# Optimization experiments

Measured on AMD Instinct MI355X. Metric: run time of the kernel, lower is better.

## Reference

```python
import jax, jax.numpy as jnp
import numpy as np

IN_CH = 64
EMBED = 128
OUT_CH = 64
NUM_HEADS = 2
HEAD_DIM = EMBED // NUM_HEADS
B, D, H, W = 2, 16, 16, 16
SEQ = D * H * W


def setup_inputs() -> dict:
    key = jax.random.key(0)
    ks = jax.random.split(key, 12)
    s = lambda fan_in: 1.0 / np.sqrt(fan_in)
    return {
        "x": jax.random.normal(ks[0], (B, IN_CH, D, H, W), dtype=jnp.float32),
        "W_cp": jax.random.uniform(ks[1], (EMBED, IN_CH), jnp.float32, -s(IN_CH), s(IN_CH)),
        "b_cp": jax.random.uniform(ks[2], (EMBED,), jnp.float32, -s(IN_CH), s(IN_CH)),
        "W_q": jax.random.uniform(ks[3], (EMBED, EMBED), jnp.float32, -s(EMBED), s(EMBED)),
        "W_k": jax.random.uniform(ks[4], (EMBED, EMBED), jnp.float32, -s(EMBED), s(EMBED)),
        "W_v": jax.random.uniform(ks[5], (EMBED, EMBED), jnp.float32, -s(EMBED), s(EMBED)),
        "W_o": jax.random.uniform(ks[6], (EMBED, EMBED), jnp.float32, -s(EMBED), s(EMBED)),
        "b_o": jax.random.uniform(ks[7], (EMBED,), jnp.float32, -s(EMBED), s(EMBED)),
        "W_out": jax.random.uniform(ks[8], (OUT_CH, EMBED), jnp.float32, -s(EMBED), s(EMBED)),
        "b_out": jax.random.uniform(ks[9], (OUT_CH,), jnp.float32, -s(EMBED), s(EMBED)),
        "pos": jax.random.normal(ks[10], (1, SEQ, EMBED), dtype=jnp.float32) * 0.02,
        "gate": jnp.float32(0.1),
    }


def reference(x, W_cp, b_cp, W_q, W_k, W_v, W_o, b_o, W_out, b_out, pos, gate):
    b, c, d, h, w = x.shape
    seq = d * h * w
    scale = HEAD_DIM ** (-0.5)
    # (B, C, D, H, W) -> (B, S, C)
    xf = jnp.transpose(x, (0, 2, 3, 4, 1)).reshape(b, seq, c)
    xf = xf @ W_cp.T + b_cp + pos  # (B, S, E)
    # QKV projections, split heads: (B, nh, S, hd)
    def heads(t):
        return jnp.transpose(t.reshape(b, seq, NUM_HEADS, HEAD_DIM), (0, 2, 1, 3))
    q = heads(xf @ W_q.T)
    k = heads(xf @ W_k.T)
    v = heads(xf @ W_v.T)
    attn = jax.nn.softmax(jnp.einsum("bnsd,bntd->bnst", q, k) * scale, axis=-1)
    o = jnp.einsum("bnst,bntd->bnsd", attn, v)  # (B, nh, S, hd)
    o = jnp.transpose(o, (0, 2, 1, 3)).reshape(b, seq, EMBED)
    o = o @ W_o.T + b_o
    o = o @ W_out.T + b_out  # (B, S, out)
    out = jnp.transpose(o, (0, 2, 1)).reshape(b, OUT_CH, d, h, w)
    # in_channels == output_dim -> skip is identity (no conv/BN in original)
    return out + gate * x
```

## Files before the change

### kernel.cpp

```cpp
#include <hip/hip_runtime.h>
#include <hip/hip_bf16.h>
#include <cstdint>

typedef unsigned short u16;
typedef __attribute__((ext_vector_type(8))) short short8;
typedef __attribute__((ext_vector_type(8))) float f32x8;
typedef __attribute__((ext_vector_type(4))) float f32x4;

#define MFMA(a, b, c) __builtin_amdgcn_mfma_f32_16x16x32_bf16((a), (b), (c), 0, 0, 0)

#define SEQ 4096
#define KSPLIT 8
#define NTILE (SEQ / KSPLIT / 32)

static __device__ __forceinline__ float b2f(u16 u) {
    union { float f; uint32_t i; } c; c.i = ((uint32_t)u) << 16; return c.f;
}
static __device__ __forceinline__ u16 f2b(float f) {
    union { float f; uint32_t i; } c; c.f = f;
    uint32_t r = c.i + 0x7FFF + ((c.i >> 16) & 1);
    return (u16)(r >> 16);
}
static __device__ __forceinline__ short8 ld8(const u16* p) {
    return *reinterpret_cast<const short8*>(p);
}
static __device__ __forceinline__ uint32_t pk2(float a, float b) {
    uint32_t r;
    asm("v_cvt_pk_bf16_f32 %0, %1, %2" : "=v"(r) : "v"(a), "v"(b));
    return r;
}
static __device__ __forceinline__ void gld16(const u16* g, u16* l) {
    __builtin_amdgcn_global_load_lds(
        (const __attribute__((address_space(1))) unsigned int*)g,
        (__attribute__((address_space(3))) unsigned int*)l, 16, 0, 0);
}

__global__ void k_prep(const float* __restrict__ Wo, const float* __restrict__ bo,
                       const float* __restrict__ Wout, const float* __restrict__ bout,
                       const float* __restrict__ Wcp, const float* __restrict__ Wq,
                       const float* __restrict__ Wk, const float* __restrict__ Wv,
                       u16* __restrict__ Wc, float* __restrict__ bc,
                       u16* __restrict__ Wcp_b, u16* __restrict__ Wq_b,
                       u16* __restrict__ Wk_b, u16* __restrict__ Wv_b) {
    int idx = blockIdx.x * 256 + threadIdx.x;
    if (idx < 8192) {
        int co = idx >> 7, e = idx & 127;
        float s = 0.f;
        for (int k = 0; k < 128; k++)
            s += Wout[co * 128 + k] * Wo[k * 128 + e];
        Wc[idx] = f2b(s);
    } else if (idx < 8256) {
        int co = idx - 8192;
        float s = bout[co];
        for (int k = 0; k < 128; k++)
            s += bo[k] * Wout[co * 128 + k];
        bc[co] = s;
    } else if (idx < 16448) {
        int i = idx - 8256;  Wcp_b[i] = f2b(Wcp[i]);
    } else if (idx < 32832) {
        int i = idx - 16448; Wq_b[i] = f2b(Wq[i]);
    } else if (idx < 49216) {
        int i = idx - 32832; Wk_b[i] = f2b(Wk[i]);
    } else if (idx < 65600) {
        int i = idx - 49216; Wv_b[i] = f2b(Wv[i]);
    }
}

__global__ __launch_bounds__(256) void k_front(const float* __restrict__ x,
                                               const u16* __restrict__ Wcp,
                                               const float* __restrict__ bcp,
                                               const float* __restrict__ pos,
                                               const u16* __restrict__ Wq,
                                               const u16* __restrict__ Wk,
                                               const u16* __restrict__ Wv,
                                               u16* __restrict__ Q, u16* __restrict__ K,
                                               u16* __restrict__ V) {
    __shared__ __align__(16) u16 xT[32][72];
    __shared__ __align__(16) u16 xfl[32 * 128];
    int blk = blockIdx.x;
    int b = blk >> 7, sb = (blk & 127) * 32;
    int t = threadIdx.x, w = t >> 6, l = t & 63, lc = l & 15, lg = l >> 4;

    {
        int c = t & 63, so = t >> 6;
        const float* src = x + ((size_t)b * 64 + c) * SEQ + sb + so * 8;
        f32x8 a0 = *reinterpret_cast<const f32x8*>(src);
#pragma unroll
        for (int j = 0; j < 8; j++) xT[so * 8 + j][c] = f2b(a0[j]);
    }
    __syncthreads();

    {
        int rt = w >> 1, eh = w & 1;
        short8 af[2];
        af[0] = ld8(&xT[rt * 16 + lc][lg * 8]);
        af[1] = ld8(&xT[rt * 16 + lc][32 + lg * 8]);
#pragma unroll
        for (int et = 0; et < 4; et++) {
            int nt = eh * 4 + et;
            f32x4 acc = {0.f, 0.f, 0.f, 0.f};
#pragma unroll
            for (int ks = 0; ks < 2; ks++) {
                short8 bfr = ld8(Wcp + (nt * 16 + lc) * 64 + ks * 32 + lg * 8);
                acc = MFMA(af[ks], bfr, acc);
            }
            int e = nt * 16 + lc;
            float be = bcp[e];
            int chunk = e >> 3;
#pragma unroll
            for (int r = 0; r < 4; r++) {
                int sl = rt * 16 + lg * 4 + r;
                float v = acc[r] + be + pos[(size_t)(sb + sl) * 128 + e];
                xfl[sl * 128 + ((chunk ^ (sl & 7)) << 3) + (e & 7)] = f2b(v);
            }
        }
    }
    __syncthreads();

    {
        int st = w & 1, hr = w >> 1;
        short8 afq[4];
#pragma unroll
        for (int ks = 0; ks < 4; ks++)
            afq[ks] = ld8(&xfl[(st * 16 + lc) * 128 + (((ks * 4 + lg) ^ (lc & 7)) << 3)]);

        const float qscl = 0.18033688011112042f;
#pragma unroll
        for (int qk = 0; qk < 2; qk++) {
            const u16* W = qk ? Wk : Wq;
            u16* dst = qk ? K : Q;
#pragma unroll
            for (int et = 0; et < 4; et++) {
                int nt = hr * 4 + et;
                f32x4 acc = {0.f, 0.f, 0.f, 0.f};
#pragma unroll
                for (int ks = 0; ks < 4; ks++) {
                    short8 bfr = ld8(W + (nt * 16 + lc) * 128 + ks * 32 + lg * 8);
                    acc = MFMA(afq[ks], bfr, acc);
                }
                int e = nt * 16 + lc, h = e >> 6, d = e & 63;
                float scl = qk ? 1.0f : qscl;
#pragma unroll
                for (int r = 0; r < 4; r++) {
                    int sr = sb + st * 16 + lg * 4 + r;
                    dst[(((size_t)b * 2 + h) * SEQ + sr) * 64 + d] = f2b(acc[r] * scl);
                }
            }
        }
#pragma unroll
        for (int et = 0; et < 4; et++) {
            int nt = hr * 4 + et;
            f32x4 acc = {0.f, 0.f, 0.f, 0.f};
            short8 wv[4];
#pragma unroll
            for (int ks = 0; ks < 4; ks++)
                wv[ks] = ld8(Wv + (nt * 16 + lc) * 128 + ks * 32 + lg * 8);
#pragma unroll
            for (int ks = 0; ks < 4; ks++)
                acc = MFMA(wv[ks], afq[ks], acc);
#pragma unroll
            for (int r = 0; r < 4; r++) {
                int d = nt * 16 + lg * 4 + r, h = d >> 6, dd = d & 63;
                V[((size_t)(b * 2 + h) * 64 + dd) * SEQ + sb + st * 16 + lc] = f2b(acc[r]);
            }
        }
    }
}

__global__ __launch_bounds__(256, 4) void k_attn(const u16* __restrict__ Q,
                                                 const u16* __restrict__ K,
                                                 const u16* __restrict__ Vg,
                                                 u16* __restrict__ Op,
                                                 float2* __restrict__ ml) {
    __shared__ __align__(16) u16 Klds[2][2048];
    __shared__ __align__(16) u16 Vlds[2][2048];
    __shared__ __align__(16) u16 Pl[4][32][32];
    int blk = blockIdx.x;
    int split = blk >> 7, bh = (blk >> 5) & 3, qb = (blk & 31) * 128;
    int kbase = split * (SEQ / KSPLIT);
    const u16* Qp = Q + (size_t)bh * SEQ * 64;
    const u16* Kp = K + (size_t)bh * SEQ * 64;
    const u16* Vp = Vg + (size_t)bh * SEQ * 64;
    int t = threadIdx.x, w = t >> 6, l = t & 63, lc = l & 15, lg = l >> 4;
    uint32_t* plw = (uint32_t*)&Pl[w][0][0];
    const u16* plu = &Pl[w][0][0];

    const u16* kSrc = Kp + (size_t)(kbase + w * 8 + (l >> 3)) * 64 + (((l & 7) ^ (l >> 3)) << 3);
    int vrow = w * 16 + (l >> 2);
    int vswz = (l & 3) ^ ((((l >> 2) & 3) + (l >> 4)) & 3);
    const u16* vSrc = Vp + (size_t)vrow * SEQ + kbase + (vswz << 3);

    short8 qa[2][2];
#pragma unroll
    for (int ks = 0; ks < 2; ks++)
#pragma unroll
        for (int qh = 0; qh < 2; qh++)
            qa[ks][qh] = ld8(Qp + (size_t)(qb + w * 32 + qh * 16 + lc) * 64 + ks * 32 + lg * 8);

    short8 onesb;
#pragma unroll
    for (int i = 0; i < 8; i++) onesb[i] = (short)0x3F80;

    f32x4 oacc[2][4], lsacc[2];
#pragma unroll
    for (int qh = 0; qh < 2; qh++) {
        lsacc[qh] = (f32x4){0.f, 0.f, 0.f, 0.f};
#pragma unroll
        for (int dt = 0; dt < 4; dt++) oacc[qh][dt] = (f32x4){0.f, 0.f, 0.f, 0.f};
    }
    float m[2] = {-INFINITY, -INFINITY};

    int c0 = (lg ^ (lc & 7)) * 8;
    int sp = (((lc & 3) + (lc >> 2)) & 3);
    int cv = (lg ^ sp) * 8;

#define STAGE(buf, tt) do {                                       \
        gld16(kSrc + (size_t)(tt) * 2048, &Klds[buf][w * 512]);   \
        gld16(vSrc + (tt) * 32,           &Vlds[buf][w * 512]);   \
    } while (0)

    STAGE(0, 0);
    __syncthreads();

#pragma unroll 2
    for (int tt = 0; tt < NTILE; tt++) {
        int cur = tt & 1;
        if (tt + 1 < NTILE) STAGE(cur ^ 1, tt + 1);

        const u16* kb = Klds[cur];
        const u16* vb = Vlds[cur];

        f32x4 sc[2][2];
#pragma unroll
        for (int nt = 0; nt < 2; nt++) {
            short8 kf0 = ld8(kb + (nt * 16 + lc) * 64 + c0);
            short8 kf1 = ld8(kb + (nt * 16 + lc) * 64 + (c0 ^ 32));
#pragma unroll
            for (int qh = 0; qh < 2; qh++) {
                f32x4 a = {0.f, 0.f, 0.f, 0.f};
                a = MFMA(kf0, qa[0][qh], a);
                a = MFMA(kf1, qa[1][qh], a);
                sc[nt][qh] = a;
            }
        }

        float mx[2];
#pragma unroll
        for (int qh = 0; qh < 2; qh++)
            mx[qh] = fmaxf(
                fmaxf(fmaxf(sc[0][qh][0], sc[0][qh][1]), fmaxf(sc[0][qh][2], sc[0][qh][3])),
                fmaxf(fmaxf(sc[1][qh][0], sc[1][qh][1]), fmaxf(sc[1][qh][2], sc[1][qh][3])));

        if (__any((mx[0] - m[0] > 8.f) || (mx[1] - m[1] > 8.f))) {
#pragma unroll
            for (int qh = 0; qh < 2; qh++) {
                float mr = fmaxf(mx[qh], __shfl_xor(mx[qh], 16));
                mr = fmaxf(mr, __shfl_xor(mr, 32));
                float mn = fmaxf(m[qh], mr);
                float corr = exp2f(m[qh] - mn);
#pragma unroll
                for (int r = 0; r < 4; r++) {
                    float cr = __shfl(corr, lg * 4 + r);
#pragma unroll
                    for (int dt = 0; dt < 4; dt++) oacc[qh][dt][r] *= cr;
                    lsacc[qh][r] *= cr;
                }
                m[qh] = mn;
            }
        }

#pragma unroll
        for (int qh = 0; qh < 2; qh++) {
            int rowb = (qh * 16 + lc) * 16 + (lg & 1) * 2;
#pragma unroll
            for (int nt = 0; nt < 2; nt++) {
                uint2 u;
                u.x = pk2(exp2f(sc[nt][qh][0] - m[qh]), exp2f(sc[nt][qh][1] - m[qh]));
                u.y = pk2(exp2f(sc[nt][qh][2] - m[qh]), exp2f(sc[nt][qh][3] - m[qh]));
                int cc = (nt * 2 + (lg >> 1)) ^ sp;
                *reinterpret_cast<uint2*>(&plw[rowb + cc * 4]) = u;
            }
        }

        short8 pa0 = ld8(plu + (lc) * 32 + cv);
        short8 pa1 = ld8(plu + (16 + lc) * 32 + cv);
        lsacc[0] = MFMA(pa0, onesb, lsacc[0]);
        lsacc[1] = MFMA(pa1, onesb, lsacc[1]);
#pragma unroll
        for (int dt = 0; dt < 4; dt++) {
            short8 vf = ld8(vb + (dt * 16 + lc) * 32 + cv);
            oacc[0][dt] = MFMA(pa0, vf, oacc[0][dt]);
            oacc[1][dt] = MFMA(pa1, vf, oacc[1][dt]);
        }
        __syncthreads();
    }
#undef STAGE

    size_t rowbase = (size_t)(split * 4 + bh) * SEQ + qb + w * 32;
#pragma unroll
    for (int qh = 0; qh < 2; qh++)
#pragma unroll
        for (int dt = 0; dt < 4; dt++)
#pragma unroll
            for (int r = 0; r < 4; r++)
                Op[(rowbase + qh * 16 + lg * 4 + r) * 64 + dt * 16 + lc] = f2b(oacc[qh][dt][r]);
    float mr[2][4];
#pragma unroll
    for (int qh = 0; qh < 2; qh++)
#pragma unroll
        for (int r = 0; r < 4; r++) mr[qh][r] = __shfl(m[qh], lg * 4 + r);
    if (lc == 0) {
#pragma unroll
        for (int qh = 0; qh < 2; qh++)
#pragma unroll
            for (int r = 0; r < 4; r++) {
                float2 v; v.x = mr[qh][r]; v.y = lsacc[qh][r];
                ml[rowbase + qh * 16 + lg * 4 + r] = v;
            }
    }
}

__global__ __launch_bounds__(256) void k_back(const u16* __restrict__ Op,
                                              const float2* __restrict__ ml,
                                              const u16* __restrict__ Wc,
                                              const float* __restrict__ bc,
                                              const float* __restrict__ x,
                                              const float* __restrict__ gate,
                                              float* __restrict__ out) {
    __shared__ __align__(16) u16 Ol[32 * 128];
    int blk = blockIdx.x;
    int b = blk >> 7, sb = (blk & 127) * 32;
    int t = threadIdx.x, w = t >> 6, l = t & 63, lc = l & 15, lg = l >> 4;
    float g = gate[0];

    {
        int sl = t >> 3, ci = t & 7;
        int h = ci >> 2, d0 = (ci & 3) * 16;
        size_t rp0 = ((size_t)(b * 2 + h) << 12) + sb + sl;
        float2 e[KSPLIT];
        float ms = -INFINITY;
#pragma unroll
        for (int k = 0; k < KSPLIT; k++) {
            e[k] = ml[rp0 + (size_t)k * 16384];
            ms = fmaxf(ms, e[k].x);
        }
        float den = 0.f, c[KSPLIT];
#pragma unroll
        for (int k = 0; k < KSPLIT; k++) {
            c[k] = exp2f(e[k].x - ms);
            den += c[k] * e[k].y;
        }
        float inv = 1.0f / den;
#pragma unroll
        for (int half = 0; half < 2; half++) {
            float acc[8];
#pragma unroll
            for (int j = 0; j < 8; j++) acc[j] = 0.f;
#pragma unroll
            for (int k = 0; k < KSPLIT; k++) {
                short8 a = ld8(Op + (rp0 + (size_t)k * 16384) * 64 + d0 + half * 8);
#pragma unroll
                for (int j = 0; j < 8; j++) acc[j] += c[k] * b2f((u16)a[j]);
            }
            short8 ov;
#pragma unroll
            for (int j = 0; j < 8; j++) ov[j] = (short)f2b(acc[j] * inv);
            int chunk = ci * 2 + half;
            *reinterpret_cast<short8*>(&Ol[sl * 128 + ((chunk ^ (sl & 7)) << 3)]) = ov;
        }
    }
    __syncthreads();

    short8 af[4];
#pragma unroll
    for (int ks = 0; ks < 4; ks++)
        af[ks] = ld8(Wc + (w * 16 + lc) * 128 + ks * 32 + lg * 8);

#pragma unroll
    for (int st = 0; st < 2; st++) {
        f32x4 acc = {0.f, 0.f, 0.f, 0.f};
#pragma unroll
        for (int ks = 0; ks < 4; ks++) {
            short8 bfr = ld8(&Ol[(st * 16 + lc) * 128 + (((ks * 4 + lg) ^ (lc & 7)) << 3)]);
            acc = MFMA(af[ks], bfr, acc);
        }
#pragma unroll
        for (int r = 0; r < 4; r++) {
            int co = w * 16 + lg * 4 + r;
            int s = sb + st * 16 + lc;
            size_t idx = ((size_t)b * 64 + co) * SEQ + s;
            out[idx] = acc[r] + bc[co] + g * x[idx];
        }
    }
}

extern "C" void kernel_launch(void* const* d_in, const int* in_sizes, int n_in,
                              void* d_out, int out_size, void* d_ws, size_t ws_size,
                              hipStream_t stream) {
    const float* x    = (const float*)d_in[0];
    const float* Wcp  = (const float*)d_in[1];
    const float* bcp  = (const float*)d_in[2];
    const float* Wq   = (const float*)d_in[3];
    const float* Wk   = (const float*)d_in[4];
    const float* Wv   = (const float*)d_in[5];
    const float* Wo   = (const float*)d_in[6];
    const float* bo   = (const float*)d_in[7];
    const float* Wout = (const float*)d_in[8];
    const float* bout = (const float*)d_in[9];
    const float* pos  = (const float*)d_in[10];
    const float* gate = (const float*)d_in[11];

    char* ws = (char*)d_ws;
    float2* mlp  = (float2*)(ws);
    u16*    Qb   = (u16*)(ws + (2u << 20));
    u16*    Kb   = (u16*)(ws + (4u << 20));
    u16*    Vt   = (u16*)(ws + (6u << 20));
    u16*    Wc   = (u16*)(ws + (10u << 20));
    float*  bc   = (float*)(ws + (10u << 20) + 16384);
    u16*    Wcp_b = (u16*)(ws + (10u << 20) + 32768);
    u16*    Wq_b  = (u16*)(ws + (10u << 20) + 49152);
    u16*    Wk_b  = (u16*)(ws + (10u << 20) + 81920);
    u16*    Wv_b  = (u16*)(ws + (10u << 20) + 114688);
    u16*    Opb  = (u16*)(ws + (10u << 20) + (512u << 10));
    float* out = (float*)d_out;

    hipLaunchKernelGGL(k_prep, dim3(257), dim3(256), 0, stream,
                       Wo, bo, Wout, bout, Wcp, Wq, Wk, Wv,
                       Wc, bc, Wcp_b, Wq_b, Wk_b, Wv_b);
    hipLaunchKernelGGL(k_front, dim3(256), dim3(256), 0, stream,
                       x, Wcp_b, bcp, pos, Wq_b, Wk_b, Wv_b, Qb, Kb, Vt);
    hipLaunchKernelGGL(k_attn, dim3(1024), dim3(256), 0, stream, Qb, Kb, Vt, Opb, mlp);
    hipLaunchKernelGGL(k_back, dim3(256), dim3(256), 0, stream, Opb, mlp, Wc, bc, x, gate, out);
}
```

Before: 60.47 us.

## Software-pipeline attention loop: overlap next tile's QK with current tile's PV

Restructures the flash-attention inner loop so each iteration computes QK^T scores for tile i+1 while doing the P·V product for tile i. The softmax exp for tile i+1 then runs after those matrix ops. K and V loads are now prefetched two tiles ahead, with V triple-buffered in LDS, and MFMA sections are wrapped in s_setprio to favour matrix issue. The goal is to hide exp/max latency and LDS/global load latency behind MFMA work. The cost is more LDS and more live registers, which could reduce occupancy. The barrier may also already wait on all outstanding loads, which would limit the gain from prefetching deeper.

Measured after the change: 62.28 us. +3.0%, slower.

```diff
diff --git a/kernel.cpp b/kernel.cpp
--- a/kernel.cpp
+++ b/kernel.cpp
@@ -173,7 +173,7 @@
                                                  u16* __restrict__ Op,
                                                  float2* __restrict__ ml) {
     __shared__ __align__(16) u16 Klds[2][2048];
-    __shared__ __align__(16) u16 Vlds[2][2048];
+    __shared__ __align__(16) u16 Vlds[3][2048];
     __shared__ __align__(16) u16 Pl[4][32][32];
     int blk = blockIdx.x;
     int split = blk >> 7, bh = (blk >> 5) & 3, qb = (blk & 31) * 128;
@@ -214,87 +214,89 @@
     int sp = (((lc & 3) + (lc >> 2)) & 3);
     int cv = (lg ^ sp) * 8;
 
-#define STAGE(buf, tt) do {                                       \
-        gld16(kSrc + (size_t)(tt) * 2048, &Klds[buf][w * 512]);   \
-        gld16(vSrc + (tt) * 32,           &Vlds[buf][w * 512]);   \
-    } while (0)
-
-    STAGE(0, 0);
+    gld16(kSrc, &Klds[0][w * 512]);
+    gld16(vSrc, &Vlds[0][w * 512]);
     __syncthreads();
 
-#pragma unroll 2
-    for (int tt = 0; tt < NTILE; tt++) {
-        int cur = tt & 1;
-        if (tt + 1 < NTILE) STAGE(cur ^ 1, tt + 1);
-
-        const u16* kb = Klds[cur];
-        const u16* vb = Vlds[cur];
-
-        f32x4 sc[2][2];
-#pragma unroll
-        for (int nt = 0; nt < 2; nt++) {
-            short8 kf0 = ld8(kb + (nt * 16 + lc) * 64 + c0);
-            short8 kf1 = ld8(kb + (nt * 16 + lc) * 64 + (c0 ^ 32));
+    f32x4 sc[2][2];
+    for (int i = -1; i < NTILE; i++) {
+        if (i + 2 < NTILE) {
+            gld16(kSrc + (size_t)(i + 2) * 2048, &Klds[(i + 2) & 1][w * 512]);
+            gld16(vSrc + (i + 2) * 32,           &Vlds[(i + 2) % 3][w * 512]);
+        }
+        if (i + 1 < NTILE) {
+            const u16* kb = Klds[(i + 1) & 1];
+            __builtin_amdgcn_s_setprio(1);
+#pragma unroll
+            for (int nt = 0; nt < 2; nt++) {
+                short8 kf0 = ld8(kb + (nt * 16 + lc) * 64 + c0);
+                short8 kf1 = ld8(kb + (nt * 16 + lc) * 64 + (c0 ^ 32));
+#pragma unroll
+                for (int qh = 0; qh < 2; qh++) {
+                    f32x4 a = {0.f, 0.f, 0.f, 0.f};
+                    a = MFMA(kf0, qa[0][qh], a);
+                    a = MFMA(kf1, qa[1][qh], a);
+                    sc[nt][qh] = a;
+                }
+            }
+            __builtin_amdgcn_s_setprio(0);
+        }
+        if (i >= 0) {
+            const u16* vb = Vlds[i % 3];
+            short8 pa0 = ld8(plu + lc * 32 + cv);
+            short8 pa1 = ld8(plu + (16 + lc) * 32 + cv);
+            __builtin_amdgcn_s_setprio(1);
+            lsacc[0] = MFMA(pa0, onesb, lsacc[0]);
+            lsacc[1] = MFMA(pa1, onesb, lsacc[1]);
+#pragma unroll
+            for (int dt = 0; dt < 4; dt++) {
+                short8 vf = ld8(vb + (dt * 16 + lc) * 32 + cv);
+                oacc[0][dt] = MFMA(pa0, vf, oacc[0][dt]);
+                oacc[1][dt] = MFMA(pa1, vf, oacc[1][dt]);
+            }
+            __builtin_amdgcn_s_setprio(0);
+        }
+        if (i + 1 < NTILE) {
+            float mx[2];
+#pragma unroll
+            for (int qh = 0; qh < 2; qh++)
+                mx[qh] = fmaxf(
+                    fmaxf(fmaxf(sc[0][qh][0], sc[0][qh][1]), fmaxf(sc[0][qh][2], sc[0][qh][3])),
+                    fmaxf(fmaxf(sc[1][qh][0], sc[1][qh][1]), fmaxf(sc[1][qh][2], sc[1][qh][3])));
+
+            if (__any((mx[0] - m[0] > 8.f) || (mx[1] - m[1] > 8.f))) {
+#pragma unroll
+                for (int qh = 0; qh < 2; qh++) {
+                    float mr = fmaxf(mx[qh], __shfl_xor(mx[qh], 16));
+                    mr = fmaxf(mr, __shfl_xor(mr, 32));
+                    float mn = fmaxf(m[qh], mr);
+                    float corr = exp2f(m[qh] - mn);
+#pragma unroll
+                    for (int r = 0; r < 4; r++) {
+                        float cr = __shfl(corr, lg * 4 + r);
+#pragma unroll
+                        for (int dt = 0; dt < 4; dt++) oacc[qh][dt][r] *= cr;
+                        lsacc[qh][r] *= cr;
+                    }
+                    m[qh] = mn;
+                }
+            }
+
 #pragma unroll
             for (int qh = 0; qh < 2; qh++) {
-                f32x4 a = {0.f, 0.f, 0.f, 0.f};
-                a = MFMA(kf0, qa[0][qh], a);
-                a = MFMA(kf1, qa[1][qh], a);
-                sc[nt][qh] = a;
-            }
-        }
-
-        float mx[2];
-#pragma unroll
-        for (int qh = 0; qh < 2; qh++)
-            mx[qh] = fmaxf(
-                fmaxf(fmaxf(sc[0][qh][0], sc[0][qh][1]), fmaxf(sc[0][qh][2], sc[0][qh][3])),
-                fmaxf(fmaxf(sc[1][qh][0], sc[1][qh][1]), fmaxf(sc[1][qh][2], sc[1][qh][3])));
-
-        if (__any((mx[0] - m[0] > 8.f) || (mx[1] - m[1] > 8.f))) {
-#pragma unroll
-            for (int qh = 0; qh < 2; qh++) {
-                float mr = fmaxf(mx[qh], __shfl_xor(mx[qh], 16));
-                mr = fmaxf(mr, __shfl_xor(mr, 32));
-                float mn = fmaxf(m[qh], mr);
-                float corr = exp2f(m[qh] - mn);
-#pragma unroll
-                for (int r = 0; r < 4; r++) {
-                    float cr = __shfl(corr, lg * 4 + r);
-#pragma unroll
-                    for (int dt = 0; dt < 4; dt++) oacc[qh][dt][r] *= cr;
-                    lsacc[qh][r] *= cr;
+                int rowb = (qh * 16 + lc) * 16 + (lg & 1) * 2;
+#pragma unroll
+                for (int nt = 0; nt < 2; nt++) {
+                    uint2 u;
+                    u.x = pk2(exp2f(sc[nt][qh][0] - m[qh]), exp2f(sc[nt][qh][1] - m[qh]));
+                    u.y = pk2(exp2f(sc[nt][qh][2] - m[qh]), exp2f(sc[nt][qh][3] - m[qh]));
+                    int cc = (nt * 2 + (lg >> 1)) ^ sp;
+                    *reinterpret_cast<uint2*>(&plw[rowb + cc * 4]) = u;
                 }
-                m[qh] = mn;
-            }
-        }
-
-#pragma unroll
-        for (int qh = 0; qh < 2; qh++) {
-            int rowb = (qh * 16 + lc) * 16 + (lg & 1) * 2;
-#pragma unroll
-            for (int nt = 0; nt < 2; nt++) {
-                uint2 u;
-                u.x = pk2(exp2f(sc[nt][qh][0] - m[qh]), exp2f(sc[nt][qh][1] - m[qh]));
-                u.y = pk2(exp2f(sc[nt][qh][2] - m[qh]), exp2f(sc[nt][qh][3] - m[qh]));
-                int cc = (nt * 2 + (lg >> 1)) ^ sp;
-                *reinterpret_cast<uint2*>(&plw[rowb + cc * 4]) = u;
-            }
-        }
-
-        short8 pa0 = ld8(plu + (lc) * 32 + cv);
-        short8 pa1 = ld8(plu + (16 + lc) * 32 + cv);
-        lsacc[0] = MFMA(pa0, onesb, lsacc[0]);
-        lsacc[1] = MFMA(pa1, onesb, lsacc[1]);
-#pragma unroll
-        for (int dt = 0; dt < 4; dt++) {
-            short8 vf = ld8(vb + (dt * 16 + lc) * 32 + cv);
-            oacc[0][dt] = MFMA(pa0, vf, oacc[0][dt]);
-            oacc[1][dt] = MFMA(pa1, vf, oacc[1][dt]);
+            }
         }
         __syncthreads();
     }
-#undef STAGE
 
     size_t rowbase = (size_t)(split * 4 + bh) * SEQ + qb + w * 32;
 #pragma unroll
```
